# Performance work log

Hardware: AMD Instinct MI355X
Metric: run time of the kernel (lower is better)

The kernel has to match this reference:

```python
import jax, jax.numpy as jnp
import numpy as np

B, C, H, W = 32, 512, 32, 32
C8 = C // 8


def setup_inputs() -> dict:
    key = jax.random.key(0)
    ks = jax.random.split(key, 4)
    x = jax.random.normal(ks[0], (B, C, W, H), dtype=jnp.float32)
    # 1x1 conv weights == channel-mixing matrices [out_c, in_c]
    Wq = jax.random.normal(ks[1], (C8, C), dtype=jnp.float32) * (1.0 / np.sqrt(C))
    Wk = jax.random.normal(ks[2], (C8, C), dtype=jnp.float32) * (1.0 / np.sqrt(C))
    Wv = jax.random.normal(ks[3], (C, C), dtype=jnp.float32) * (1.0 / np.sqrt(C))
    bq = jnp.zeros((C8,), jnp.float32)
    bk = jnp.zeros((C8,), jnp.float32)
    bv = jnp.zeros((C,), jnp.float32)
    alpha = jnp.float32(1.0)  # nonzero so attention path is exercised
    return {"x": x, "Wq": Wq, "bq": bq, "Wk": Wk, "bk": bk, "Wv": Wv, "bv": bv, "alpha": alpha}


def reference(x, Wq, bq, Wk, bk, Wv, bv, alpha):
    b, c, w, h = x.shape
    n = w * h
    xf = x.reshape(b, c, n)  # [B, C, N]
    # 1x1 convs = per-pixel channel GEMMs
    q = jnp.einsum('oc,bcn->bon', Wq, xf) + bq[None, :, None]  # [B, C8, N]
    k = jnp.einsum('oc,bcn->bon', Wk, xf) + bk[None, :, None]  # [B, C8, N]
    v = jnp.einsum('oc,bcn->bon', Wv, xf) + bv[None, :, None]  # [B, C,  N]
    # energy[b, n, m] = q[:, n] . k[:, m]  (unscaled, full attention)
    energy = jnp.einsum('bcn,bcm->bnm', q, k)  # [B, N, N]
    attention = jax.nn.softmax(energy, axis=-1)
    # out[b, c, n] = sum_m v[b, c, m] * attention[b, n, m]
    out = jnp.einsum('bcm,bnm->bcn', v, attention)
    out = out.reshape(b, c, w, h)
    return alpha * out + x
```

## Files before the change

### kernel.cpp

```cpp
#include <hip/hip_runtime.h>
#include <math.h>

#define B_DIM  32
#define C_DIM  512
#define N_DIM  1024
#define LOG2E  1.44269504088896340736f
#define NEG_BIG (-1.0e30f)

typedef __attribute__((ext_vector_type(8))) __bf16 bf16x8;
typedef __attribute__((ext_vector_type(8))) short short8v;
typedef __attribute__((ext_vector_type(4))) short short4v;
typedef __attribute__((ext_vector_type(4))) float floatx4;

__device__ __forceinline__ unsigned short f2bf(float f) {
    unsigned u = __float_as_uint(f);
    return (unsigned short)((u + 0x7FFFu + ((u >> 16) & 1u)) >> 16);
}
__device__ __forceinline__ float bf2f(unsigned short h) {
    return __uint_as_float(((unsigned)h) << 16);
}
__device__ __forceinline__ floatx4 mfma16(short8v a, short8v b, floatx4 c) {
    return __builtin_amdgcn_mfma_f32_16x16x32_bf16(
        __builtin_bit_cast(bf16x8, a), __builtin_bit_cast(bf16x8, b), c, 0, 0, 0);
}
__device__ __forceinline__ float fin(float v) {
    return (__builtin_fabsf(v) <= 1.0e30f) ? v : 0.0f;
}

__global__ __launch_bounds__(256) void tx2_kernel(
    const float* __restrict__ x,
    unsigned short* __restrict__ xth, unsigned short* __restrict__ xtl)
{
    __shared__ float tile[64][65];
    const int n0 = blockIdx.x * 64, c0 = blockIdx.y * 64, b = blockIdx.z;
    const int t = threadIdx.x;

    #pragma unroll
    for (int p = 0; p < 4; ++p) {
        const int r = (t >> 4) + 16 * p;
        const float4 v = *(const float4*)(x + ((size_t)b*C_DIM + c0 + r)*N_DIM
                                          + n0 + (t & 15)*4);
        tile[r][(t&15)*4+0] = v.x;  tile[r][(t&15)*4+1] = v.y;
        tile[r][(t&15)*4+2] = v.z;  tile[r][(t&15)*4+3] = v.w;
    }
    __syncthreads();
    #pragma unroll
    for (int p = 0; p < 2; ++p) {
        const int rn = (t >> 3) + 32 * p;
        const int c8 = (t & 7) * 8;
        short8v hi, lo;
        #pragma unroll
        for (int j = 0; j < 8; ++j) {
            const float f = tile[c8 + j][rn];
            const unsigned short h = f2bf(f);
            hi[j] = (short)h;
            lo[j] = (short)f2bf(f - bf2f(h));
        }
        const size_t base = ((size_t)b*N_DIM + n0 + rn)*C_DIM + c0 + c8;
        *(short8v*)(xth + base) = hi;
        *(short8v*)(xtl + base) = lo;
    }
}

__global__ __launch_bounds__(256) void qkproj_mfma(
    const unsigned short* __restrict__ xth, const unsigned short* __restrict__ xtl,
    const float* __restrict__ Wq, const float* __restrict__ bq,
    const float* __restrict__ Wk, const float* __restrict__ bk,
    unsigned short* __restrict__ qkt)
{
    __shared__ unsigned short Ah[128][40], Al[128][40];
    __shared__ unsigned short Bh[128][40], Bl[128][40];
    const int b = blockIdx.z, n0 = blockIdx.x * 128;
    const int t = threadIdx.x, w = t >> 6, l = t & 63;
    const int la = l & 15, lb = l >> 4;
    const int nh = (w & 1) * 64, oh = (w >> 1) * 64;

    floatx4 acc[4][4];
    #pragma unroll
    for (int i = 0; i < 4; ++i)
        #pragma unroll
        for (int j = 0; j < 4; ++j) acc[i][j] = (floatx4)0.0f;

    for (int k0 = 0; k0 < C_DIM; k0 += 32) {
        #pragma unroll
        for (int p = 0; p < 2; ++p) {
            const int idx = t + 256*p, row = idx >> 2, ch = idx & 3;
            const size_t g = ((size_t)b*N_DIM + n0 + row)*C_DIM + k0 + ch*8;
            *(short8v*)&Ah[row][ch*8] = *(const short8v*)(xth + g);
            *(short8v*)&Al[row][ch*8] = *(const short8v*)(xtl + g);
        }
        #pragma unroll
        for (int p = 0; p < 4; ++p) {
            const int idx = t + 256*p, row = idx >> 3, ch = idx & 7;
            const float* Wrow = (row < 64) ? (Wq + (size_t)row * C_DIM)
                                           : (Wk + (size_t)(row - 64) * C_DIM);
            const float4 wv = *(const float4*)(Wrow + k0 + ch*4);
            const float fv[4] = {wv.x, wv.y, wv.z, wv.w};
            short4v sh, sl;
            #pragma unroll
            for (int j = 0; j < 4; ++j) {
                const unsigned short h = f2bf(fv[j]);
                sh[j] = (short)h;
                sl[j] = (short)f2bf(fv[j] - bf2f(h));
            }
            *(short4v*)&Bh[row][ch*4] = sh;
            *(short4v*)&Bl[row][ch*4] = sl;
        }
        __syncthreads();

        short8v ahf[4], alf[4], bhf[4], blf[4];
        #pragma unroll
        for (int nt = 0; nt < 4; ++nt) {
            ahf[nt] = *(const short8v*)&Ah[nh + nt*16 + la][lb*8];
            alf[nt] = *(const short8v*)&Al[nh + nt*16 + la][lb*8];
        }
        #pragma unroll
        for (int ot = 0; ot < 4; ++ot) {
            bhf[ot] = *(const short8v*)&Bh[oh + ot*16 + la][lb*8];
            blf[ot] = *(const short8v*)&Bl[oh + ot*16 + la][lb*8];
        }
        #pragma unroll
        for (int nt = 0; nt < 4; ++nt)
            #pragma unroll
            for (int ot = 0; ot < 4; ++ot) {
                acc[nt][ot] = mfma16(ahf[nt], bhf[ot], acc[nt][ot]);
                acc[nt][ot] = mfma16(ahf[nt], blf[ot], acc[nt][ot]);
                acc[nt][ot] = mfma16(alf[nt], bhf[ot], acc[nt][ot]);
            }
        __syncthreads();
    }

    const int plane = (oh == 0) ? 0 : 2;
    #pragma unroll
    for (int ot = 0; ot < 4; ++ot) {
        const int o = oh + ot*16 + la;
        const int c = o & 63;
        const float bias = (oh == 0) ? bq[o] : bk[o - 64];
        #pragma unroll
        for (int nt = 0; nt < 4; ++nt)
            #pragma unroll
            for (int r = 0; r < 4; ++r) {
                const int n = n0 + nh + nt*16 + lb*4 + r;
                const float f = acc[nt][ot][r] + bias;
                const unsigned short h = f2bf(f);
                const unsigned short lo16 = f2bf(f - bf2f(h));
                qkt[(((size_t)b*4 + plane    )*N_DIM + n)*64 + c] = h;
                qkt[(((size_t)b*4 + plane + 1)*N_DIM + n)*64 + c] = lo16;
            }
    }
}

__global__ __launch_bounds__(256) void vproj_mfma(
    const unsigned short* __restrict__ xt,
    const float* __restrict__ Wv, const float* __restrict__ bvv,
    unsigned short* __restrict__ vbf)
{
    __shared__ unsigned short Axs[128][40];
    __shared__ unsigned short Bws[128][40];
    const int b = blockIdx.z, m0 = blockIdx.x * 128, c0 = blockIdx.y * 128;
    const int t = threadIdx.x, w = t >> 6, l = t & 63;
    const int la = l & 15, lb = l >> 4;
    const int mh = (w & 1) * 64, chh = (w >> 1) * 64;

    floatx4 acc[4][4];
    #pragma unroll
    for (int i = 0; i < 4; ++i)
        #pragma unroll
        for (int j = 0; j < 4; ++j) acc[i][j] = (floatx4)0.0f;

    for (int k0 = 0; k0 < C_DIM; k0 += 32) {
        #pragma unroll
        for (int p = 0; p < 2; ++p) {
            const int idx = t + 256 * p;
            const int row = idx >> 2, ch = idx & 3;
            *(short8v*)&Axs[row][ch*8] =
                *(const short8v*)(xt + ((size_t)b*N_DIM + m0 + row)*C_DIM + k0 + ch*8);
        }
        #pragma unroll
        for (int p = 0; p < 4; ++p) {
            const int idx = t + 256 * p;
            const int row = idx >> 3, ch = idx & 7;
            const float4 wv = *(const float4*)(Wv + (size_t)(c0 + row)*C_DIM + k0 + ch*4);
            short4v s;
            s[0] = (short)f2bf(wv.x); s[1] = (short)f2bf(wv.y);
            s[2] = (short)f2bf(wv.z); s[3] = (short)f2bf(wv.w);
            *(short4v*)&Bws[row][ch*4] = s;
        }
        __syncthreads();
        short8v af[4], bfv[4];
        #pragma unroll
        for (int mt = 0; mt < 4; ++mt)
            af[mt] = *(const short8v*)&Axs[mh + mt*16 + la][lb*8];
        #pragma unroll
        for (int ct = 0; ct < 4; ++ct)
            bfv[ct] = *(const short8v*)&Bws[chh + ct*16 + la][lb*8];
        #pragma unroll
        for (int mt = 0; mt < 4; ++mt)
            #pragma unroll
            for (int ct = 0; ct < 4; ++ct)
                acc[mt][ct] = mfma16(af[mt], bfv[ct], acc[mt][ct]);
        __syncthreads();
    }
    #pragma unroll
    for (int ct = 0; ct < 4; ++ct) {
        const int c = c0 + chh + ct*16 + la;
        const float bias = bvv[c];
        #pragma unroll
        for (int mt = 0; mt < 4; ++mt) {
            const int m = m0 + mh + mt*16 + lb*4;
            short4v s;
            #pragma unroll
            for (int r = 0; r < 4; ++r) s[r] = (short)f2bf(acc[mt][ct][r] + bias);
            *(short4v*)(vbf + ((size_t)b*C_DIM + c)*N_DIM + m) = s;
        }
    }
}

__global__ __launch_bounds__(256) void attn_mfma(
    const unsigned short* __restrict__ qkt,
    const unsigned short* __restrict__ vbf,
    const float* __restrict__ x,
    const float* __restrict__ alpha_p,
    float* __restrict__ out)
{
    __shared__ unsigned short Qh[32][72], Ql[32][72];
    __shared__ unsigned short Kh[64][72], Kl[64][72];
    __shared__ __align__(16) float S[32][68];
    __shared__ unsigned short Pb[32][72];
    __shared__ float row_m[32], row_l[32], row_scale[32];

    const int id  = blockIdx.x;
    const int lin = (id & 7) * 128 + (id >> 3);
    const int b   = lin >> 5;
    const int n0  = (lin & 31) * 32;

    const int t = threadIdx.x, w = t >> 6, l = t & 63;
    const int la = l & 15, lb = l >> 4;
    const unsigned short* qkb = qkt + (size_t)b * 4 * N_DIM * 64;

    #pragma unroll
    for (int plane = 0; plane < 2; ++plane) {
        const int row = t >> 3;
        const int ch  = t & 7;
        const short8v g = *(const short8v*)(qkb + ((size_t)plane*N_DIM + n0 + row)*64 + ch*8);
        if (plane == 0) *(short8v*)&Qh[row][ch*8] = g;
        else            *(short8v*)&Ql[row][ch*8] = g;
    }
    if (t < 32) { row_m[t] = NEG_BIG; row_l[t] = 0.0f; row_scale[t] = 1.0f; }
    __syncthreads();

    floatx4 acc[2][8];
    #pragma unroll
    for (int i = 0; i < 2; ++i)
        #pragma unroll
        for (int j = 0; j < 8; ++j) acc[i][j] = (floatx4)0.0f;

    #pragma unroll 1
    for (int m0 = 0; m0 < N_DIM; m0 += 64) {
        #pragma unroll
        for (int pp = 0; pp < 4; ++pp) {
            const int plane = pp >> 1;
            const int idx   = t + 256 * (pp & 1);
            const int row   = idx >> 3;
            const int ch    = idx & 7;
            const short8v g = *(const short8v*)(qkb + ((size_t)(2 + plane)*N_DIM + m0 + row)*64 + ch*8);
            if (plane == 0) *(short8v*)&Kh[row][ch*8] = g;
            else            *(short8v*)&Kl[row][ch*8] = g;
        }
        __syncthreads();

        {
            floatx4 e[2] = { (floatx4)0.0f, (floatx4)0.0f };
            #pragma unroll
            for (int ks = 0; ks < 2; ++ks) {
                const short8v ah = *(const short8v*)&Kh[w*16 + la][ks*32 + lb*8];
                const short8v al = *(const short8v*)&Kl[w*16 + la][ks*32 + lb*8];
                #pragma unroll
                for (int nt = 0; nt < 2; ++nt) {
                    const short8v bh = *(const short8v*)&Qh[nt*16 + la][ks*32 + lb*8];
                    const short8v bl = *(const short8v*)&Ql[nt*16 + la][ks*32 + lb*8];
                    e[nt] = mfma16(ah, bh, e[nt]);
                    e[nt] = mfma16(ah, bl, e[nt]);
                    e[nt] = mfma16(al, bh, e[nt]);
                }
            }
            #pragma unroll
            for (int nt = 0; nt < 2; ++nt) {
                floatx4 ev = e[nt];
                #pragma unroll
                for (int r = 0; r < 4; ++r) ev[r] = fin(ev[r]);
                *(floatx4*)&S[nt*16 + la][w*16 + lb*4] = ev;
            }
        }
        __syncthreads();

        {
            const int row = t >> 3, seg = t & 7;
            const float4 sa = *(const float4*)&S[row][seg*8];
            const float4 sb = *(const float4*)&S[row][seg*8 + 4];
            float mx = fmaxf(fmaxf(fmaxf(sa.x,sa.y), fmaxf(sa.z,sa.w)),
                             fmaxf(fmaxf(sb.x,sb.y), fmaxf(sb.z,sb.w)));
            mx = fmaxf(mx, __shfl_xor(mx, 1));
            mx = fmaxf(mx, __shfl_xor(mx, 2));
            mx = fmaxf(mx, __shfl_xor(mx, 4));
            const float m_old = row_m[row];
            const float m_new = fmaxf(m_old, mx);
            const float p0 = exp2f((sa.x - m_new) * LOG2E);
            const float p1 = exp2f((sa.y - m_new) * LOG2E);
            const float p2 = exp2f((sa.z - m_new) * LOG2E);
            const float p3 = exp2f((sa.w - m_new) * LOG2E);
            const float p4 = exp2f((sb.x - m_new) * LOG2E);
            const float p5 = exp2f((sb.y - m_new) * LOG2E);
            const float p6 = exp2f((sb.z - m_new) * LOG2E);
            const float p7 = exp2f((sb.w - m_new) * LOG2E);
            float sum = ((p0+p1)+(p2+p3)) + ((p4+p5)+(p6+p7));
            sum += __shfl_xor(sum, 1);
            sum += __shfl_xor(sum, 2);
            sum += __shfl_xor(sum, 4);
            short8v pk;
            pk[0]=(short)f2bf(p0); pk[1]=(short)f2bf(p1);
            pk[2]=(short)f2bf(p2); pk[3]=(short)f2bf(p3);
            pk[4]=(short)f2bf(p4); pk[5]=(short)f2bf(p5);
            pk[6]=(short)f2bf(p6); pk[7]=(short)f2bf(p7);
            *(short8v*)&Pb[row][seg*8] = pk;
            if (seg == 0) {
                const float sc = exp2f((m_old - m_new) * LOG2E);
                row_scale[row] = sc;
                row_l[row] = row_l[row] * sc + sum;
                row_m[row] = m_new;
            }
        }
        __syncthreads();

        {
            float fsc[2][4];
            #pragma unroll
            for (int nt = 0; nt < 2; ++nt)
                #pragma unroll
                for (int r = 0; r < 4; ++r) fsc[nt][r] = row_scale[nt*16 + lb*4 + r];
            #pragma unroll
            for (int nt = 0; nt < 2; ++nt)
                #pragma unroll
                for (int ct = 0; ct < 8; ++ct)
                    #pragma unroll
                    for (int r = 0; r < 4; ++r) acc[nt][ct][r] *= fsc[nt][r];
        }

        #pragma unroll
        for (int ks = 0; ks < 2; ++ks) {
            short8v pa[2];
            #pragma unroll
            for (int nt = 0; nt < 2; ++nt)
                pa[nt] = *(const short8v*)&Pb[nt*16 + la][ks*32 + lb*8];
            const unsigned short* vp =
                vbf + ((size_t)b*C_DIM + w*128 + la)*N_DIM + m0 + ks*32 + lb*8;
            #pragma unroll
            for (int ct = 0; ct < 8; ++ct) {
                const short8v bv8 = *(const short8v*)(vp + (size_t)ct*16*N_DIM);
                acc[0][ct] = mfma16(pa[0], bv8, acc[0][ct]);
                acc[1][ct] = mfma16(pa[1], bv8, acc[1][ct]);
            }
        }
        __syncthreads();
    }

    const float alpha = alpha_p[0];
    float invl[2][4];
    #pragma unroll
    for (int nt = 0; nt < 2; ++nt)
        #pragma unroll
        for (int r = 0; r < 4; ++r)
            invl[nt][r] = alpha / fmaxf(row_l[nt*16 + lb*4 + r], 1.0e-20f);
    #pragma unroll
    for (int nt = 0; nt < 2; ++nt)
        #pragma unroll
        for (int ct = 0; ct < 8; ++ct) {
            const int c = w*128 + ct*16 + la;
            const size_t base = ((size_t)b*C_DIM + c)*N_DIM + n0 + nt*16 + lb*4;
            const float4 xa = *(const float4*)&x[base];
            float4 o;
            o.x = fmaf(fin(acc[nt][ct][0]), invl[nt][0], xa.x);
            o.y = fmaf(fin(acc[nt][ct][1]), invl[nt][1], xa.y);
            o.z = fmaf(fin(acc[nt][ct][2]), invl[nt][2], xa.z);
            o.w = fmaf(fin(acc[nt][ct][3]), invl[nt][3], xa.w);
            *(float4*)&out[base] = o;
        }
}

extern "C" void kernel_launch(void* const* d_in, const int* in_sizes, int n_in,
                              void* d_out, int out_size, void* d_ws, size_t ws_size,
                              hipStream_t stream)
{
    const float* x     = (const float*)d_in[0];
    const float* Wq    = (const float*)d_in[1];
    const float* bq    = (const float*)d_in[2];
    const float* Wk    = (const float*)d_in[3];
    const float* bk    = (const float*)d_in[4];
    const float* Wv    = (const float*)d_in[5];
    const float* bv    = (const float*)d_in[6];
    const float* alpha = (const float*)d_in[7];
    float* out = (float*)d_out;

    unsigned short* xth = (unsigned short*)d_ws;
    unsigned short* xtl = (unsigned short*)((char*)d_ws + ((size_t)32 << 20));
    unsigned short* vbf = xtl;
    unsigned short* qkt = (unsigned short*)((char*)d_ws + ((size_t)64 << 20));

    tx2_kernel <<<dim3(16, 8, B_DIM), 256, 0, stream>>>(x, xth, xtl);
    qkproj_mfma<<<dim3(8, 1, B_DIM), 256, 0, stream>>>(xth, xtl, Wq, bq, Wk, bk, qkt);
    vproj_mfma <<<dim3(8, 4, B_DIM), 256, 0, stream>>>(xth, Wv, bv, vbf);
    attn_mfma  <<<dim3(B_DIM * 32), 256, 0, stream>>>(qkt, vbf, x, alpha, out);
}
```

Before: 444.8 us.

## Prefetch next K tile and current V tile into registers in attention loop

Restructures the attention loop so the next K tile is loaded into registers at the start of each iteration and stored to LDS only after the PV MFMAs. The V fragments for the current tile are also loaded up front, so global-memory latency overlaps the QK and softmax phases. Plain __syncthreads are replaced by a barrier that waits only on LDS counters, and launch bounds request 2 blocks per CU. The register prefetch (vreg is 16 short8v) raises register pressure, which may cause spills under the new occupancy bound.

```diff
diff --git a/kernel.cpp b/kernel.cpp
--- a/kernel.cpp
+++ b/kernel.cpp
@@ -26,6 +26,12 @@
 __device__ __forceinline__ float fin(float v) {
     return (__builtin_fabsf(v) <= 1.0e30f) ? v : 0.0f;
 }
+
+#define BAR_LDS()  do {                                            \
+    asm volatile("s_waitcnt lgkmcnt(0)" ::: "memory");             \
+    __builtin_amdgcn_s_barrier();                                  \
+    asm volatile("" ::: "memory");                                 \
+} while (0)
 
 __global__ __launch_bounds__(256) void tx2_kernel(
     const float* __restrict__ x,
@@ -216,7 +222,7 @@
     }
 }
 
-__global__ __launch_bounds__(256) void attn_mfma(
+__global__ __launch_bounds__(256, 2) void attn_mfma(
     const unsigned short* __restrict__ qkt,
     const unsigned short* __restrict__ vbf,
     const float* __restrict__ x,
@@ -246,6 +252,16 @@
         if (plane == 0) *(short8v*)&Qh[row][ch*8] = g;
         else            *(short8v*)&Ql[row][ch*8] = g;
     }
+    #pragma unroll
+    for (int pp = 0; pp < 4; ++pp) {
+        const int plane = pp >> 1;
+        const int idx   = t + 256 * (pp & 1);
+        const int row   = idx >> 3;
+        const int ch    = idx & 7;
+        const short8v g = *(const short8v*)(qkb + ((size_t)(2 + plane)*N_DIM + row)*64 + ch*8);
+        if (plane == 0) *(short8v*)&Kh[row][ch*8] = g;
+        else            *(short8v*)&Kl[row][ch*8] = g;
+    }
     if (t < 32) { row_m[t] = NEG_BIG; row_l[t] = 0.0f; row_scale[t] = 1.0f; }
     __syncthreads();
 
@@ -256,18 +272,28 @@
         for (int j = 0; j < 8; ++j) acc[i][j] = (floatx4)0.0f;
 
     #pragma unroll 1
-    for (int m0 = 0; m0 < N_DIM; m0 += 64) {
+    for (int it = 0; it < 16; ++it) {
+        const int m0  = it * 64;
+        const int m0n = (it < 15) ? (m0 + 64) : 0;
+
+        short8v vreg[2][8];
+        #pragma unroll
+        for (int ks = 0; ks < 2; ++ks) {
+            const unsigned short* vp =
+                vbf + ((size_t)b*C_DIM + w*128 + la)*N_DIM + m0 + ks*32 + lb*8;
+            #pragma unroll
+            for (int ct = 0; ct < 8; ++ct)
+                vreg[ks][ct] = *(const short8v*)(vp + (size_t)ct*16*N_DIM);
+        }
+        short8v kreg[4];
         #pragma unroll
         for (int pp = 0; pp < 4; ++pp) {
             const int plane = pp >> 1;
             const int idx   = t + 256 * (pp & 1);
             const int row   = idx >> 3;
             const int ch    = idx & 7;
-            const short8v g = *(const short8v*)(qkb + ((size_t)(2 + plane)*N_DIM + m0 + row)*64 + ch*8);
-            if (plane == 0) *(short8v*)&Kh[row][ch*8] = g;
-            else            *(short8v*)&Kl[row][ch*8] = g;
-        }
-        __syncthreads();
+            kreg[pp] = *(const short8v*)(qkb + ((size_t)(2 + plane)*N_DIM + m0n + row)*64 + ch*8);
+        }
 
         {
             floatx4 e[2] = { (floatx4)0.0f, (floatx4)0.0f };
@@ -292,7 +318,7 @@
                 *(floatx4*)&S[nt*16 + la][w*16 + lb*4] = ev;
             }
         }
-        __syncthreads();
+        BAR_LDS();
 
         {
             const int row = t >> 3, seg = t & 7;
@@ -330,7 +356,7 @@
                 row_m[row] = m_new;
             }
         }
-        __syncthreads();
+        BAR_LDS();
 
         {
             float fsc[2][4];
@@ -345,23 +371,28 @@
                     #pragma unroll
                     for (int r = 0; r < 4; ++r) acc[nt][ct][r] *= fsc[nt][r];
         }
-
         #pragma unroll
         for (int ks = 0; ks < 2; ++ks) {
-            short8v pa[2];
-            #pragma unroll
-            for (int nt = 0; nt < 2; ++nt)
-                pa[nt] = *(const short8v*)&Pb[nt*16 + la][ks*32 + lb*8];
-            const unsigned short* vp =
-                vbf + ((size_t)b*C_DIM + w*128 + la)*N_DIM + m0 + ks*32 + lb*8;
+            const short8v pa0 = *(const short8v*)&Pb[la][ks*32 + lb*8];
+            const short8v pa1 = *(const short8v*)&Pb[16 + la][ks*32 + lb*8];
             #pragma unroll
             for (int ct = 0; ct < 8; ++ct) {
-                const short8v bv8 = *(const short8v*)(vp + (size_t)ct*16*N_DIM);
-                acc[0][ct] = mfma16(pa[0], bv8, acc[0][ct]);
-                acc[1][ct] = mfma16(pa[1], bv8, acc[1][ct]);
-            }
-        }
-        __syncthreads();
+                acc[0][ct] = mfma16(pa0, vreg[ks][ct], acc[0][ct]);
+                acc[1][ct] = mfma16(pa1, vreg[ks][ct], acc[1][ct]);
+            }
+        }
+        BAR_LDS();
+
+        #pragma unroll
+        for (int pp = 0; pp < 4; ++pp) {
+            const int plane = pp >> 1;
+            const int idx   = t + 256 * (pp & 1);
+            const int row   = idx >> 3;
+            const int ch    = idx & 7;
+            if (plane == 0) *(short8v*)&Kh[row][ch*8] = kreg[pp];
+            else            *(short8v*)&Kl[row][ch*8] = kreg[pp];
+        }
+        BAR_LDS();
     }
 
     const float alpha = alpha_p[0];
```

After: 371.0 us. 1.2x faster.
